# Performance work log

Hardware: AMD Instinct MI355X
Metric: run time of the kernel (lower is better)

## Reference

```python
import jax, jax.numpy as jnp
import numpy as np

K = 512
RATE = 0.999

def _l2norm(v):
    # matches torch F.normalize(dim=1): v / max(||v||, 1e-12)
    n = jnp.linalg.norm(v, axis=1, keepdims=True)
    return v / jnp.maximum(n, 1e-12)

def setup_inputs() -> dict:
    key = jax.random.key(0)
    k1, k2 = jax.random.split(key)
    x = jax.random.normal(k1, (16, 256, 64, 64), dtype=jnp.float32)
    m = jax.random.normal(k2, (K, 256), dtype=jnp.float32)
    return {"x": x, "m": m}

def reference(x, m):
    b, c, h, w = x.shape
    xf = x.transpose(0, 2, 3, 1).reshape(-1, c)          # (n, c)
    xn = _l2norm(xf)
    mn = _l2norm(m)
    score = xn @ mn.T                                     # (n, k)
    # EMA codebook update (uses detached x in the original)
    xd = jax.lax.stop_gradient(xf)
    embed_ind = jnp.argmax(score, axis=1)                 # (n,)
    embed_sum = jax.ops.segment_sum(xd, embed_ind, num_segments=K)   # (k, c)
    counts = jax.ops.segment_sum(jnp.ones(xd.shape[0], xd.dtype), embed_ind, num_segments=K)
    embed_mean = embed_sum / (counts[:, None] + 1e-6)
    new_m = m * RATE + embed_mean * (1.0 - RATE)          # (k, c)
    # re-score against updated codebook
    mn2 = _l2norm(new_m)
    score2 = xn @ mn2.T                                   # (n, k)
    soft_label = jax.nn.softmax(score2, axis=1)
    out = soft_label @ new_m                              # (n, c)
    out = out.reshape(b, h, w, c).transpose(0, 3, 1, 2)   # (b, c, h, w)
    return out, score2
```

## Files before the change

kernel.cpp:

```cpp
#include <hip/hip_runtime.h>

#define Bb 16
#define Cc 256
#define HW 4096
#define Nn 65536
#define Kk 512

typedef __attribute__((ext_vector_type(4))) float f32x4;
typedef __attribute__((ext_vector_type(8))) short short8;

__device__ __forceinline__ float bf2f(unsigned int u){
  union { float f; unsigned int i; } v; v.i = u << 16; return v.f;
}
__device__ __forceinline__ unsigned short f2bf(float f){
  unsigned int i = __float_as_uint(f);
  unsigned int r = (i + 0x7fffu + ((i >> 16) & 1u)) >> 16;
  return (unsigned short)r;
}

__global__ __launch_bounds__(64) void k_mnorm(const float* __restrict__ m,
                                              unsigned short* __restrict__ mn){
  int k = blockIdx.x, l = threadIdx.x;
  float4 v = *reinterpret_cast<const float4*>(m + (size_t)k * Cc + l * 4);
  float ss = v.x*v.x + v.y*v.y + v.z*v.z + v.w*v.w;
  #pragma unroll
  for (int off = 1; off < 64; off <<= 1) ss += __shfl_xor(ss, off, 64);
  float rn = 1.0f / fmaxf(sqrtf(ss), 1e-12f);
  ushort4 o;
  o.x = f2bf(v.x*rn); o.y = f2bf(v.y*rn); o.z = f2bf(v.z*rn); o.w = f2bf(v.w*rn);
  *reinterpret_cast<ushort4*>(mn + (size_t)k * Cc + l * 4) = o;
}

__global__ __launch_bounds__(512, 4) void k_prep_score(const float* __restrict__ x,
                                                       const unsigned short* __restrict__ mn,
                                                       float* __restrict__ rs,
                                                       unsigned short* __restrict__ xr,
                                                       int* __restrict__ eind){
  __shared__ __align__(16) char ldsB[32768];
  __shared__ float red[8][64];
  __shared__ float smax[8][64];
  __shared__ int   sidx[8][64];
  int t = threadIdx.x, w = t >> 6, l = t & 63, gr = l >> 4, li = l & 15;
  int b = blockIdx.x >> 6;
  int hw0 = (blockIdx.x & 63) << 6;
  const float* src = x + ((size_t)b * Cc + w * 32) * HW + hw0 + l;
  float ss = 0.f;
  unsigned int pk[16];
  #pragma unroll
  for (int j = 0; j < 16; ++j){
    float v0 = src[(size_t)(2*j    ) * HW];
    float v1 = src[(size_t)(2*j + 1) * HW];
    ss += v0 * v0 + v1 * v1;
    pk[j] = (unsigned int)f2bf(v0) | ((unsigned int)f2bf(v1) << 16);
  }
  #pragma unroll
  for (int q = 0; q < 4; ++q){
    int colb = w * 64 + q * 16;
    int4 vv;
    vv.x = (int)pk[q*4+0]; vv.y = (int)pk[q*4+1];
    vv.z = (int)pk[q*4+2]; vv.w = (int)pk[q*4+3];
    *reinterpret_cast<int4*>(ldsB + l * 512 + (colb ^ ((l & 7) << 4))) = vv;
  }
  red[w][l] = ss;
  __syncthreads();
  if (t < 64){
    float s = 0.f;
    #pragma unroll
    for (int ww = 0; ww < 8; ++ww) s += red[ww][t];
    rs[(size_t)b * HW + hw0 + t] = 1.0f / fmaxf(sqrtf(s), 1e-12f);
  }
  f32x4 acc[4][4];
  #pragma unroll
  for (int mt = 0; mt < 4; ++mt)
    #pragma unroll
    for (int nt = 0; nt < 4; ++nt)
      acc[mt][nt] = (f32x4){0.f,0.f,0.f,0.f};
  const short* mnp = reinterpret_cast<const short*>(mn);
  for (int ks = 0; ks < 8; ++ks){
    short8 af[4];
    #pragma unroll
    for (int mt = 0; mt < 4; ++mt){
      int row = mt * 16 + li;
      af[mt] = *reinterpret_cast<const short8*>(
          ldsB + row * 512 + ((ks * 64 + gr * 16) ^ ((row & 7) << 4)));
    }
    #pragma unroll
    for (int nt = 0; nt < 4; ++nt){
      short8 bv = *reinterpret_cast<const short8*>(
          mnp + (size_t)(w * 64 + nt * 16 + li) * Cc + ks * 32 + gr * 8);
      #pragma unroll
      for (int mt = 0; mt < 4; ++mt)
        acc[mt][nt] = __builtin_amdgcn_mfma_f32_16x16x32_bf16(af[mt], bv, acc[mt][nt], 0, 0, 0);
    }
  }
  #pragma unroll
  for (int mt = 0; mt < 4; ++mt){
    #pragma unroll
    for (int r = 0; r < 4; ++r){
      float best = acc[mt][0][r]; int bi = w * 64 + li;
      #pragma unroll
      for (int nt = 1; nt < 4; ++nt){
        float v = acc[mt][nt][r]; int ii = w * 64 + nt * 16 + li;
        if (v > best){ best = v; bi = ii; }
      }
      #pragma unroll
      for (int off = 1; off < 16; off <<= 1){
        float ov = __shfl_xor(best, off, 64);
        int   oi = __shfl_xor(bi,   off, 64);
        if (ov > best || (ov == best && oi < bi)){ best = ov; bi = oi; }
      }
      if (li == 0){ int pr = mt * 16 + gr * 4 + r; smax[w][pr] = best; sidx[w][pr] = bi; }
    }
  }
  __syncthreads();
  if (t < 64){
    float best = smax[0][t]; int bi = sidx[0][t];
    #pragma unroll
    for (int ww = 1; ww < 8; ++ww){
      float v = smax[ww][t]; int ii = sidx[ww][t];
      if (v > best || (v == best && ii < bi)){ best = v; bi = ii; }
    }
    eind[(size_t)b * HW + hw0 + t] = bi;
  }
  char* dst = reinterpret_cast<char*>(xr) + ((size_t)b * HW + hw0) * 512;
  #pragma unroll
  for (int i = 0; i < 4; ++i){
    int px = i * 16 + (t >> 5);
    int colb = (t & 31) * 16;
    int4 rv = *reinterpret_cast<const int4*>(ldsB + px * 512 + (colb ^ ((px & 7) << 4)));
    *reinterpret_cast<int4*>(dst + (size_t)px * 512 + colb) = rv;
  }
}

__global__ __launch_bounds__(256) void k_segsum(const int* __restrict__ eind,
                                                const unsigned short* __restrict__ xr,
                                                float* __restrict__ es4,
                                                float* __restrict__ ec4){
  int kk = blockIdx.x >> 2, qr = blockIdx.x & 3;
  int t = threadIdx.x, w = t >> 6, l = t & 63;
  float a0=0.f,a1=0.f,a2=0.f,a3=0.f;
  int cnt = 0;
  int base = qr * 16384 + w * 4096;
  for (int it = 0; it < 16; ++it){
    int pxb = base + it * 256;
    int4 e = *reinterpret_cast<const int4*>(eind + pxb + l * 4);
    #pragma unroll
    for (int comp = 0; comp < 4; ++comp){
      int ev = comp == 0 ? e.x : comp == 1 ? e.y : comp == 2 ? e.z : e.w;
      unsigned long long mask = __ballot(ev == kk);
      cnt += (int)__popcll(mask);
      while (mask){
        int src = __ffsll((unsigned long long)mask) - 1;
        mask &= mask - 1;
        int px = pxb + src * 4 + comp;
        ushort4 uv = *reinterpret_cast<const ushort4*>(xr + (size_t)px * Cc + l * 4);
        a0 += bf2f(uv.x); a1 += bf2f(uv.y);
        a2 += bf2f(uv.z); a3 += bf2f(uv.w);
      }
    }
  }
  __shared__ float red[4][256];
  __shared__ float rcnt[4];
  red[w][l*4+0]=a0; red[w][l*4+1]=a1; red[w][l*4+2]=a2; red[w][l*4+3]=a3;
  if (l == 0) rcnt[w] = (float)cnt;
  __syncthreads();
  float s = red[0][t] + red[1][t] + red[2][t] + red[3][t];
  es4[(size_t)blockIdx.x * Cc + t] = s;
  if (t == 0) ec4[blockIdx.x] = rcnt[0] + rcnt[1] + rcnt[2] + rcnt[3];
}

__global__ __launch_bounds__(64) void k_update(const float* __restrict__ es4,
                                               const float* __restrict__ ec4,
                                               const float* __restrict__ m,
                                               unsigned short* __restrict__ mn2,
                                               unsigned short* __restrict__ nmT){
  int k = blockIdx.x, l = threadIdx.x;
  float sx = 0.f, sy = 0.f, sz = 0.f, sw = 0.f, cs = 0.f;
  #pragma unroll
  for (int q = 0; q < 4; ++q){
    float4 s = *reinterpret_cast<const float4*>(es4 + ((size_t)(4*k+q)) * Cc + l * 4);
    sx += s.x; sy += s.y; sz += s.z; sw += s.w;
    cs += ec4[4*k+q];
  }
  float4 mv = *reinterpret_cast<const float4*>(m + (size_t)k * Cc + l * 4);
  float inv = 1.0f / (cs + 1e-6f);
  float nx = mv.x * 0.999f + sx * inv * 0.001f;
  float ny = mv.y * 0.999f + sy * inv * 0.001f;
  float nz = mv.z * 0.999f + sz * inv * 0.001f;
  float nw = mv.w * 0.999f + sw * inv * 0.001f;
  float ss = nx*nx + ny*ny + nz*nz + nw*nw;
  #pragma unroll
  for (int off = 1; off < 64; off <<= 1) ss += __shfl_xor(ss, off, 64);
  float rn = 1.0f / fmaxf(sqrtf(ss), 1e-12f);
  ushort4 o;
  o.x = f2bf(nx*rn); o.y = f2bf(ny*rn); o.z = f2bf(nz*rn); o.w = f2bf(nw*rn);
  *reinterpret_cast<ushort4*>(mn2 + (size_t)k * Cc + l * 4) = o;
  nmT[(size_t)(l*4+0) * Kk + k] = f2bf(nx);
  nmT[(size_t)(l*4+1) * Kk + k] = f2bf(ny);
  nmT[(size_t)(l*4+2) * Kk + k] = f2bf(nz);
  nmT[(size_t)(l*4+3) * Kk + k] = f2bf(nw);
}

__global__ __launch_bounds__(512, 4) void k_out(const unsigned short* __restrict__ xr,
                                                const float* __restrict__ rs,
                                                const unsigned short* __restrict__ mn2,
                                                const unsigned short* __restrict__ nmT,
                                                float* __restrict__ out,
                                                float* __restrict__ score2){
  __shared__ __align__(16) char smem[65536];
  __shared__ float wbuf[8 * 64];
  __shared__ float rz[64];
  __shared__ float rsl[64];
  int t = threadIdx.x, w = t >> 6, l = t & 63, gr = l >> 4, li = l & 15;
  int px0 = blockIdx.x * 64;
  const char* gsrc = reinterpret_cast<const char*>(xr + (size_t)px0 * Cc);
  #pragma unroll
  for (int j = 0; j < 4; ++j){
    int chunk = j * 512 + t;
    int rr = chunk >> 5, slot = chunk & 31;
    int4 v = *reinterpret_cast<const int4*>(gsrc + rr * 512 + slot * 16);
    *reinterpret_cast<int4*>(smem + rr * 512 + ((slot * 16) ^ ((rr & 7) << 4))) = v;
  }
  if (t < 64) rsl[t] = rs[px0 + t];
  __syncthreads();
  f32x4 acc[4][4];
  #pragma unroll
  for (int kt = 0; kt < 4; ++kt)
    #pragma unroll
    for (int pt = 0; pt < 4; ++pt)
      acc[kt][pt] = (f32x4){0.f,0.f,0.f,0.f};
  const short* mnp = reinterpret_cast<const short*>(mn2);
  int kw = w * 64;
  for (int ks = 0; ks < 8; ++ks){
    short8 am[4];
    #pragma unroll
    for (int kt = 0; kt < 4; ++kt)
      am[kt] = *reinterpret_cast<const short8*>(
          mnp + (size_t)(kw + kt * 16 + li) * Cc + ks * 32 + gr * 8);
    short8 bx[4];
    #pragma unroll
    for (int pt = 0; pt < 4; ++pt){
      int row = pt * 16 + li;
      bx[pt] = *reinterpret_cast<const short8*>(
          smem + row * 512 + ((ks * 64 + gr * 16) ^ ((row & 7) << 4)));
    }
    #pragma unroll
    for (int kt = 0; kt < 4; ++kt)
      #pragma unroll
      for (int pt = 0; pt < 4; ++pt)
        acc[kt][pt] = __builtin_amdgcn_mfma_f32_16x16x32_bf16(am[kt], bx[pt], acc[kt][pt], 0, 0, 0);
  }
  __syncthreads();
  float s[4] = {0.f, 0.f, 0.f, 0.f};
  float* s2 = score2 + (size_t)px0 * Kk;
  #pragma unroll
  for (int kt = 0; kt < 4; ++kt){
    #pragma unroll
    for (int pt = 0; pt < 4; ++pt){
      int px = pt * 16 + li;
      float rsv = rsl[px];
      f32x4 v = acc[kt][pt];
      v[0] *= rsv; v[1] *= rsv; v[2] *= rsv; v[3] *= rsv;
      *reinterpret_cast<f32x4*>(s2 + (size_t)px * Kk + kw + kt * 16 + gr * 4) = v;
      float p0 = __expf(v[0]), p1 = __expf(v[1]), p2 = __expf(v[2]), p3 = __expf(v[3]);
      s[pt] += (p0 + p1) + (p2 + p3);
      unsigned int lo = (unsigned int)f2bf(p0) | ((unsigned int)f2bf(p1) << 16);
      unsigned int hi = (unsigned int)f2bf(p2) | ((unsigned int)f2bf(p3) << 16);
      int colb = (kw + kt * 16 + gr * 4) * 2;
      uint2 pv; pv.x = lo; pv.y = hi;
      *reinterpret_cast<uint2*>(smem + px * 1024 + (colb ^ ((px & 7) << 4))) = pv;
    }
  }
  #pragma unroll
  for (int pt = 0; pt < 4; ++pt){
    s[pt] += __shfl_xor(s[pt], 16, 64);
    s[pt] += __shfl_xor(s[pt], 32, 64);
  }
  if (gr == 0){
    #pragma unroll
    for (int pt = 0; pt < 4; ++pt) wbuf[w * 64 + pt * 16 + li] = s[pt];
  }
  __syncthreads();
  if (t < 64){
    float sum = wbuf[t];
    #pragma unroll
    for (int ww = 1; ww < 8; ++ww) sum += wbuf[ww * 64 + t];
    rz[t] = 1.0f / sum;
  }
  f32x4 acc2[4][2];
  #pragma unroll
  for (int mt = 0; mt < 4; ++mt)
    #pragma unroll
    for (int nt = 0; nt < 2; ++nt)
      acc2[mt][nt] = (f32x4){0.f,0.f,0.f,0.f};
  const short* nmp = reinterpret_cast<const short*>(nmT);
  for (int ks = 0; ks < 16; ++ks){
    short8 af[4];
    #pragma unroll
    for (int mt = 0; mt < 4; ++mt){
      int row = mt * 16 + li;
      af[mt] = *reinterpret_cast<const short8*>(
          smem + row * 1024 + ((ks * 64 + gr * 16) ^ ((row & 7) << 4)));
    }
    #pragma unroll
    for (int nt = 0; nt < 2; ++nt){
      short8 bv = *reinterpret_cast<const short8*>(
          nmp + (size_t)(w * 32 + nt * 16 + li) * Kk + ks * 32 + gr * 8);
      #pragma unroll
      for (int mt = 0; mt < 4; ++mt)
        acc2[mt][nt] = __builtin_amdgcn_mfma_f32_16x16x32_bf16(af[mt], bv, acc2[mt][nt], 0, 0, 0);
    }
  }
  __syncthreads();
  int b = px0 >> 12, hw0 = px0 & 4095;
  #pragma unroll
  for (int mt = 0; mt < 4; ++mt){
    int pb = mt * 16 + gr * 4;
    float r0 = rz[pb + 0], r1 = rz[pb + 1], r2 = rz[pb + 2], r3 = rz[pb + 3];
    #pragma unroll
    for (int nt = 0; nt < 2; ++nt){
      int c = w * 32 + nt * 16 + li;
      f32x4 v;
      v[0] = acc2[mt][nt][0] * r0;
      v[1] = acc2[mt][nt][1] * r1;
      v[2] = acc2[mt][nt][2] * r2;
      v[3] = acc2[mt][nt][3] * r3;
      *reinterpret_cast<f32x4*>(out + ((size_t)b * Cc + c) * HW + hw0 + pb) = v;
    }
  }
}

extern "C" void kernel_launch(void* const* d_in, const int* in_sizes, int n_in,
                              void* d_out, int out_size, void* d_ws, size_t ws_size,
                              hipStream_t stream) {
  (void)in_sizes; (void)n_in; (void)out_size; (void)ws_size;
  const float* x = (const float*)d_in[0];
  const float* m = (const float*)d_in[1];
  float* out    = (float*)d_out;
  float* score2 = (float*)d_out + (size_t)Nn * Cc;

  char* ws = (char*)d_ws;
  unsigned short* xr  = (unsigned short*)(ws);
  float*          rsb = (float*)(ws + 33554432);
  unsigned short* mn  = (unsigned short*)(ws + 33816576);
  int*            ei  = (int*)(ws + 34078720);
  float*          es4 = (float*)(ws + 34340864);
  float*          ec4 = (float*)(ws + 36438016);
  unsigned short* mn2 = (unsigned short*)(ws + 36446208);
  unsigned short* nmT = (unsigned short*)(ws + 36708352);

  k_mnorm       <<<512,  64,  0, stream>>>(m, mn);
  k_prep_score  <<<1024, 512, 0, stream>>>(x, mn, rsb, xr, ei);
  k_segsum      <<<2048, 256, 0, stream>>>(ei, xr, es4, ec4);
  k_update      <<<512,  64,  0, stream>>>(es4, ec4, m, mn2, nmT);
  k_out         <<<1024, 512, 0, stream>>>(xr, rsb, mn2, nmT, out, score2);
}
```

Measured before the change: 182.6 us.

## Pre-swizzle codebook operands into MFMA fragment order and defer score2 stores

The normalized codebook, updated codebook and its transpose are written in a layout that matches MFMA B-fragment order. Each lane's 16-byte global load in the score and output GEMMs then falls in one contiguous 1KB block per wave instead of being spread across 16 rows. In k_out, the score2 global stores are moved after the softmax-sum barrier so they can overlap the second GEMM. The cost is a more scattered per-element write pattern in k_update and extra live registers holding the scores.

```diff
diff --git a/kernel.cpp b/kernel.cpp
--- a/kernel.cpp
+++ b/kernel.cpp
@@ -18,8 +18,9 @@
   return (unsigned short)r;
 }
 
+
 __global__ __launch_bounds__(64) void k_mnorm(const float* __restrict__ m,
-                                              unsigned short* __restrict__ mn){
+                                              unsigned short* __restrict__ mnf){
   int k = blockIdx.x, l = threadIdx.x;
   float4 v = *reinterpret_cast<const float4*>(m + (size_t)k * Cc + l * 4);
   float ss = v.x*v.x + v.y*v.y + v.z*v.z + v.w*v.w;
@@ -28,11 +29,15 @@
   float rn = 1.0f / fmaxf(sqrtf(ss), 1e-12f);
   ushort4 o;
   o.x = f2bf(v.x*rn); o.y = f2bf(v.y*rn); o.z = f2bf(v.z*rn); o.w = f2bf(v.w*rn);
-  *reinterpret_cast<ushort4*>(mn + (size_t)k * Cc + l * 4) = o;
+  int kw = k >> 6, kt = (k >> 4) & 3, li = k & 15;
+  int c0 = l * 4;
+  int ks = c0 >> 5, gr = (c0 >> 3) & 3, eo = (l & 1) * 4;
+  size_t off8 = ((((size_t)(kw*4 + kt)*8 + ks)*16 + li)*4 + gr)*8 + eo;
+  *reinterpret_cast<ushort4*>(mnf + off8) = o;
 }
 
 __global__ __launch_bounds__(512, 4) void k_prep_score(const float* __restrict__ x,
-                                                       const unsigned short* __restrict__ mn,
+                                                       const unsigned short* __restrict__ mnf,
                                                        float* __restrict__ rs,
                                                        unsigned short* __restrict__ xr,
                                                        int* __restrict__ eind){
@@ -75,7 +80,7 @@
     #pragma unroll
     for (int nt = 0; nt < 4; ++nt)
       acc[mt][nt] = (f32x4){0.f,0.f,0.f,0.f};
-  const short* mnp = reinterpret_cast<const short*>(mn);
+  int loff = li * 32 + gr * 8;
   for (int ks = 0; ks < 8; ++ks){
     short8 af[4];
     #pragma unroll
@@ -87,7 +92,7 @@
     #pragma unroll
     for (int nt = 0; nt < 4; ++nt){
       short8 bv = *reinterpret_cast<const short8*>(
-          mnp + (size_t)(w * 64 + nt * 16 + li) * Cc + ks * 32 + gr * 8);
+          mnf + ((size_t)(w*4 + nt)*8 + ks)*512 + loff);
       #pragma unroll
       for (int mt = 0; mt < 4; ++mt)
         acc[mt][nt] = __builtin_amdgcn_mfma_f32_16x16x32_bf16(af[mt], bv, acc[mt][nt], 0, 0, 0);
@@ -172,8 +177,8 @@
 __global__ __launch_bounds__(64) void k_update(const float* __restrict__ es4,
                                                const float* __restrict__ ec4,
                                                const float* __restrict__ m,
-                                               unsigned short* __restrict__ mn2,
-                                               unsigned short* __restrict__ nmT){
+                                               unsigned short* __restrict__ mn2f,
+                                               unsigned short* __restrict__ nmTf){
   int k = blockIdx.x, l = threadIdx.x;
   float sx = 0.f, sy = 0.f, sz = 0.f, sw = 0.f, cs = 0.f;
   #pragma unroll
@@ -194,17 +199,30 @@
   float rn = 1.0f / fmaxf(sqrtf(ss), 1e-12f);
   ushort4 o;
   o.x = f2bf(nx*rn); o.y = f2bf(ny*rn); o.z = f2bf(nz*rn); o.w = f2bf(nw*rn);
-  *reinterpret_cast<ushort4*>(mn2 + (size_t)k * Cc + l * 4) = o;
-  nmT[(size_t)(l*4+0) * Kk + k] = f2bf(nx);
-  nmT[(size_t)(l*4+1) * Kk + k] = f2bf(ny);
-  nmT[(size_t)(l*4+2) * Kk + k] = f2bf(nz);
-  nmT[(size_t)(l*4+3) * Kk + k] = f2bf(nw);
+  {
+    int kw = k >> 6, kt = (k >> 4) & 3, li = k & 15;
+    int c0 = l * 4;
+    int ks = c0 >> 5, gr = (c0 >> 3) & 3, eo = (l & 1) * 4;
+    size_t off8 = ((((size_t)(kw*4 + kt)*8 + ks)*16 + li)*4 + gr)*8 + eo;
+    *reinterpret_cast<ushort4*>(mn2f + off8) = o;
+  }
+  {
+    int ksn = k >> 5, grn = (k >> 3) & 3, en = k & 7;
+    unsigned short nv[4] = {f2bf(nx), f2bf(ny), f2bf(nz), f2bf(nw)};
+    #pragma unroll
+    for (int q = 0; q < 4; ++q){
+      int c = l * 4 + q;
+      int cb = c >> 4, li2 = c & 15;
+      size_t off8 = ((((size_t)cb*16 + ksn)*16 + li2)*4 + grn)*8 + en;
+      nmTf[off8] = nv[q];
+    }
+  }
 }
 
 __global__ __launch_bounds__(512, 4) void k_out(const unsigned short* __restrict__ xr,
                                                 const float* __restrict__ rs,
-                                                const unsigned short* __restrict__ mn2,
-                                                const unsigned short* __restrict__ nmT,
+                                                const unsigned short* __restrict__ mn2f,
+                                                const unsigned short* __restrict__ nmTf,
                                                 float* __restrict__ out,
                                                 float* __restrict__ score2){
   __shared__ __align__(16) char smem[65536];
@@ -229,14 +247,14 @@
     #pragma unroll
     for (int pt = 0; pt < 4; ++pt)
       acc[kt][pt] = (f32x4){0.f,0.f,0.f,0.f};
-  const short* mnp = reinterpret_cast<const short*>(mn2);
   int kw = w * 64;
+  int loff = li * 32 + gr * 8;
   for (int ks = 0; ks < 8; ++ks){
     short8 am[4];
     #pragma unroll
     for (int kt = 0; kt < 4; ++kt)
       am[kt] = *reinterpret_cast<const short8*>(
-          mnp + (size_t)(kw + kt * 16 + li) * Cc + ks * 32 + gr * 8);
+          mn2f + ((size_t)(w*4 + kt)*8 + ks)*512 + loff);
     short8 bx[4];
     #pragma unroll
     for (int pt = 0; pt < 4; ++pt){
@@ -252,7 +270,6 @@
   }
   __syncthreads();
   float s[4] = {0.f, 0.f, 0.f, 0.f};
-  float* s2 = score2 + (size_t)px0 * Kk;
   #pragma unroll
   for (int kt = 0; kt < 4; ++kt){
     #pragma unroll
@@ -261,7 +278,7 @@
       float rsv = rsl[px];
       f32x4 v = acc[kt][pt];
       v[0] *= rsv; v[1] *= rsv; v[2] *= rsv; v[3] *= rsv;
-      *reinterpret_cast<f32x4*>(s2 + (size_t)px * Kk + kw + kt * 16 + gr * 4) = v;
+      acc[kt][pt] = v;
       float p0 = __expf(v[0]), p1 = __expf(v[1]), p2 = __expf(v[2]), p3 = __expf(v[3]);
       s[pt] += (p0 + p1) + (p2 + p3);
       unsigned int lo = (unsigned int)f2bf(p0) | ((unsigned int)f2bf(p1) << 16);
@@ -282,18 +299,25 @@
   }
   __syncthreads();
   if (t < 64){
-    float sum = wbuf[t];
-    #pragma unroll
-    for (int ww = 1; ww < 8; ++ww) sum += wbuf[ww * 64 + t];
+    float sum = 0.f;
+    #pragma unroll
+    for (int ww = 0; ww < 8; ++ww) sum += wbuf[ww * 64 + t];
     rz[t] = 1.0f / sum;
   }
+  float* s2 = score2 + (size_t)px0 * Kk;
+  #pragma unroll
+  for (int kt = 0; kt < 4; ++kt)
+    #pragma unroll
+    for (int pt = 0; pt < 4; ++pt){
+      int px = pt * 16 + li;
+      *reinterpret_cast<f32x4*>(s2 + (size_t)px * Kk + kw + kt * 16 + gr * 4) = acc[kt][pt];
+    }
   f32x4 acc2[4][2];
   #pragma unroll
   for (int mt = 0; mt < 4; ++mt)
     #pragma unroll
     for (int nt = 0; nt < 2; ++nt)
       acc2[mt][nt] = (f32x4){0.f,0.f,0.f,0.f};
-  const short* nmp = reinterpret_cast<const short*>(nmT);
   for (int ks = 0; ks < 16; ++ks){
     short8 af[4];
     #pragma unroll
@@ -305,7 +329,7 @@
     #pragma unroll
     for (int nt = 0; nt < 2; ++nt){
       short8 bv = *reinterpret_cast<const short8*>(
-          nmp + (size_t)(w * 32 + nt * 16 + li) * Kk + ks * 32 + gr * 8);
+          nmTf + ((size_t)(w*2 + nt)*16 + ks)*512 + loff);
       #pragma unroll
       for (int mt = 0; mt < 4; ++mt)
         acc2[mt][nt] = __builtin_amdgcn_mfma_f32_16x16x32_bf16(af[mt], bv, acc2[mt][nt], 0, 0, 0);
@@ -316,15 +340,15 @@
   #pragma unroll
   for (int mt = 0; mt < 4; ++mt){
     int pb = mt * 16 + gr * 4;
-    float r0 = rz[pb + 0], r1 = rz[pb + 1], r2 = rz[pb + 2], r3 = rz[pb + 3];
+    f32x4 rzv = *reinterpret_cast<const f32x4*>(&rz[pb]);
     #pragma unroll
     for (int nt = 0; nt < 2; ++nt){
       int c = w * 32 + nt * 16 + li;
       f32x4 v;
-      v[0] = acc2[mt][nt][0] * r0;
-      v[1] = acc2[mt][nt][1] * r1;
-      v[2] = acc2[mt][nt][2] * r2;
-      v[3] = acc2[mt][nt][3] * r3;
+      v[0] = acc2[mt][nt][0] * rzv[0];
+      v[1] = acc2[mt][nt][1] * rzv[1];
+      v[2] = acc2[mt][nt][2] * rzv[2];
+      v[3] = acc2[mt][nt][3] * rzv[3];
       *reinterpret_cast<f32x4*>(out + ((size_t)b * Cc + c) * HW + hw0 + pb) = v;
     }
   }
@@ -340,18 +364,18 @@
   float* score2 = (float*)d_out + (size_t)Nn * Cc;
 
   char* ws = (char*)d_ws;
-  unsigned short* xr  = (unsigned short*)(ws);
-  float*          rsb = (float*)(ws + 33554432);
-  unsigned short* mn  = (unsigned short*)(ws + 33816576);
-  int*            ei  = (int*)(ws + 34078720);
-  float*          es4 = (float*)(ws + 34340864);
-  float*          ec4 = (float*)(ws + 36438016);
-  unsigned short* mn2 = (unsigned short*)(ws + 36446208);
-  unsigned short* nmT = (unsigned short*)(ws + 36708352);
-
-  k_mnorm       <<<512,  64,  0, stream>>>(m, mn);
-  k_prep_score  <<<1024, 512, 0, stream>>>(x, mn, rsb, xr, ei);
+  unsigned short* xr   = (unsigned short*)(ws);
+  float*          rsb  = (float*)(ws + 33554432);
+  unsigned short* mnf  = (unsigned short*)(ws + 33816576);
+  int*            ei   = (int*)(ws + 34078720);
+  float*          es4  = (float*)(ws + 34340864);
+  float*          ec4  = (float*)(ws + 36438016);
+  unsigned short* mn2f = (unsigned short*)(ws + 36446208);
+  unsigned short* nmTf = (unsigned short*)(ws + 36708352);
+
+  k_mnorm       <<<512,  64,  0, stream>>>(m, mnf);
+  k_prep_score  <<<1024, 512, 0, stream>>>(x, mnf, rsb, xr, ei);
   k_segsum      <<<2048, 256, 0, stream>>>(ei, xr, es4, ec4);
-  k_update      <<<512,  64,  0, stream>>>(es4, ec4, m, mn2, nmT);
-  k_out         <<<1024, 512, 0, stream>>>(xr, rsb, mn2, nmT, out, score2);
-}
+  k_update      <<<512,  64,  0, stream>>>(es4, ec4, m, mn2f, nmTf);
+  k_out         <<<1024, 512, 0, stream>>>(xr, rsb, mn2f, nmTf, out, score2);
+}
```

After: 173.9 us. 1.05x faster.
